# Kernel tuning notes

Measured on AMD Instinct MI355X. Metric: run time of the kernel, lower is better.

The kernel has to match this reference:

```python
import jax, jax.numpy as jnp
import numpy as np


def setup_inputs() -> dict:
    key = jax.random.key(0)
    ks = jax.random.split(key, 8)
    B, H, W, C = 4, 64, 64, 256
    Ck = C // 8  # key/query channels
    x = jax.random.normal(ks[0], (B, H, W, C), dtype=jnp.float32)
    Wf = jax.random.normal(ks[1], (C, Ck), dtype=jnp.float32) * (1.0 / np.sqrt(C))
    Wg = jax.random.normal(ks[2], (C, Ck), dtype=jnp.float32) * (1.0 / np.sqrt(C))
    Wh = jax.random.normal(ks[3], (C, C), dtype=jnp.float32) * (1.0 / np.sqrt(C))
    bf = jnp.zeros((Ck,), dtype=jnp.float32)
    bg = jnp.zeros((Ck,), dtype=jnp.float32)
    bh = jnp.zeros((C,), dtype=jnp.float32)
    gamma = jax.random.normal(ks[4], (), dtype=jnp.float32) * 0.1
    return {"x": x, "Wf": Wf, "bf": bf, "Wg": Wg, "bg": bg, "Wh": Wh, "bh": bh, "gamma": gamma}


def reference(x, Wf, bf, Wg, bg, Wh, bh, gamma):
    B, H, W, C = x.shape
    N = H * W
    # 1x1 convs == per-pixel matmuls over channel dim
    f = jnp.einsum('bhwc,ck->bhwk', x, Wf) + bf  # [B,H,W,C/8]
    g = jnp.einsum('bhwc,ck->bhwk', x, Wg) + bg  # [B,H,W,C/8]
    h = jnp.einsum('bhwc,cd->bhwd', x, Wh) + bh  # [B,H,W,C]
    f_flat = f.reshape(B, N, -1)
    g_flat = g.reshape(B, N, -1)
    h_flat = h.reshape(B, N, C)
    # s[b,i,j] = <g_i, f_j>   (query = g, key = f, as in the TF code)
    s = jnp.einsum('bik,bjk->bij', g_flat, f_flat)  # [B,N,N]
    b = jax.nn.softmax(s, axis=-1)
    o = jnp.einsum('bij,bjd->bid', b, h_flat)  # [B,N,C]
    y = gamma * o.reshape(B, H, W, C) + x
    return y
```

## Files before the change

kernel.cpp:

```cpp
#include <hip/hip_runtime.h>
#include <hip/hip_bf16.h>
#include <math.h>


typedef __bf16 bf16x8 __attribute__((ext_vector_type(8)));
typedef float f32x4 __attribute__((ext_vector_type(4)));

#define NPIX 4096
#define CDIM 256
#define CK   32

union U128 { unsigned int d[4]; uint4 u4; bf16x8 v; };

__device__ __forceinline__ unsigned int cvtpk(float lo, float hi) {
    unsigned int r;
    asm("v_cvt_pk_bf16_f32 %0, %1, %2" : "=v"(r) : "v"(lo), "v"(hi));
    return r;
}

__global__ __launch_bounds__(256) void prep_wtf(
    const float* __restrict__ Wf, const float* __restrict__ Wg,
    const float* __restrict__ Wh, __bf16* __restrict__ WTf)
{
    const int k = blockIdx.x;
    const int c = threadIdx.x;
    const int kk = k >> 5, kj = k & 31;
    {
        const float v = Wh[k * 256 + c];
        const int ct = 4 + (c >> 4), l15 = c & 15;
        WTf[((size_t)(ct * 8 + kk) * 16 + l15) * 32 + kj] = (__bf16)v;
    }
    if (c < 32) {
        const float v = Wf[k * 32 + c];
        const int ct = c >> 4, l15 = c & 15;
        WTf[((size_t)(ct * 8 + kk) * 16 + l15) * 32 + kj] = (__bf16)v;
    } else if (c < 64) {
        const int cc = c - 32;
        const float v = Wg[k * 32 + cc];
        const int ct = 2 + (cc >> 4), l15 = cc & 15;
        WTf[((size_t)(ct * 8 + kk) * 16 + l15) * 32 + kj] = (__bf16)v;
    }
}

__global__ __launch_bounds__(512, 1) void proj_mfma(
    const float* __restrict__ x, const __bf16* __restrict__ WTf,
    const float* __restrict__ bf_, const float* __restrict__ bg_,
    const float* __restrict__ bh_,
    __bf16* __restrict__ fbuf, __bf16* __restrict__ gbuf,
    __bf16* __restrict__ hT)
{
    __shared__ __bf16 xs[64 * 256];

    const int t = threadIdx.x;
    const int rowbase = blockIdx.x * 64;

    #pragma unroll
    for (int i = 0; i < 8; ++i) {
        const int flat = i * 2048 + t * 4;
        const int row = flat >> 8, col = flat & 255;
        const float4 xv = *(const float4*)&x[(size_t)rowbase * 256 + flat];
        const unsigned int d0 = cvtpk(xv.x, xv.y);
        const unsigned int d1 = cvtpk(xv.z, xv.w);
        const int s = (col >> 3) ^ (row & 7);
        uint2 w; w.x = d0; w.y = d1;
        *(uint2*)&xs[row * 256 + s * 8 + (col & 7)] = w;
    }
    __syncthreads();

    const int wv = t >> 6, lane = t & 63, l15 = lane & 15, lhi = lane >> 4;
    const int b = rowbase >> 12;
    const int nloc = rowbase & 4095;

    if (wv < 2) {
        const int rb0 = wv * 2;
        f32x4 acc[4][2];
        #pragma unroll
        for (int c = 0; c < 4; ++c)
            #pragma unroll
            for (int rb = 0; rb < 2; ++rb) acc[c][rb] = (f32x4){0.f, 0.f, 0.f, 0.f};
        #pragma unroll
        for (int kk = 0; kk < 8; ++kk) {
            bf16x8 xf[2];
            #pragma unroll
            for (int rb = 0; rb < 2; ++rb) {
                const int row = (rb0 + rb) * 16 + l15;
                xf[rb] = *(const bf16x8*)&xs[row * 256 + (((kk * 4 + lhi) ^ (row & 7)) * 8)];
            }
            #pragma unroll
            for (int c = 0; c < 4; ++c) {
                const bf16x8 w = *(const bf16x8*)&WTf[((size_t)(c * 8 + kk) * 16 + l15) * 32 + lhi * 8];
                acc[c][0] = __builtin_amdgcn_mfma_f32_16x16x32_bf16(xf[0], w, acc[c][0], 0, 0, 0);
                acc[c][1] = __builtin_amdgcn_mfma_f32_16x16x32_bf16(xf[1], w, acc[c][1], 0, 0, 0);
            }
        }
        #pragma unroll
        for (int c = 0; c < 4; ++c) {
            const float bia = (c < 2) ? bf_[c * 16 + l15] : bg_[(c - 2) * 16 + l15];
            __bf16* dst = (c < 2) ? fbuf : gbuf;
            const int ch = (c & 1) * 16 + l15;
            #pragma unroll
            for (int rb = 0; rb < 2; ++rb)
                #pragma unroll
                for (int r = 0; r < 4; ++r)
                    dst[(size_t)(rowbase + (rb0 + rb) * 16 + lhi * 4 + r) * CK + ch] =
                        (__bf16)(acc[c][rb][r] + bia);
        }
    } else {
        const int nct = (wv < 6) ? 3 : 2;
        const int ct0 = (wv < 6) ? (wv - 2) * 3 : 12 + (wv - 6) * 2;
        f32x4 acc[3][4];
        #pragma unroll
        for (int c = 0; c < 3; ++c)
            #pragma unroll
            for (int rb = 0; rb < 4; ++rb) acc[c][rb] = (f32x4){0.f, 0.f, 0.f, 0.f};
        #pragma unroll
        for (int kk = 0; kk < 8; ++kk) {
            bf16x8 xf[4];
            #pragma unroll
            for (int rb = 0; rb < 4; ++rb) {
                const int row = rb * 16 + l15;
                xf[rb] = *(const bf16x8*)&xs[row * 256 + (((kk * 4 + lhi) ^ (row & 7)) * 8)];
            }
            #pragma unroll
            for (int c = 0; c < 3; ++c) {
                if (c < nct) {
                    const bf16x8 w = *(const bf16x8*)
                        &WTf[((size_t)((4 + ct0 + c) * 8 + kk) * 16 + l15) * 32 + lhi * 8];
                    #pragma unroll
                    for (int rb = 0; rb < 4; ++rb)
                        acc[c][rb] = __builtin_amdgcn_mfma_f32_16x16x32_bf16(w, xf[rb], acc[c][rb], 0, 0, 0);
                }
            }
        }
        #pragma unroll
        for (int c = 0; c < 3; ++c) {
            if (c < nct) {
                #pragma unroll
                for (int r = 0; r < 4; ++r) {
                    const int ch = (ct0 + c) * 16 + lhi * 4 + r;
                    const float bia = bh_[ch];
                    #pragma unroll
                    for (int rb = 0; rb < 4; ++rb)
                        hT[((size_t)b * CDIM + ch) * NPIX + nloc + rb * 16 + l15] =
                            (__bf16)(acc[c][rb][r] + bia);
                }
            }
        }
    }
}

#define PL32(a, b) asm("v_permlane32_swap_b32 %0, %1" : "+v"(a), "+v"(b))
#define PL16(a, b) asm("v_permlane16_swap_b32 %0, %1" : "+v"(a), "+v"(b))

#define ATTN_TILE(KV, PB, FC, FN, HC, HN)                                           \
do {                                                                                \
    if (wv < 4) {                                                                   \
        const f32x4 m30 = {-30.f, -30.f, -30.f, -30.f};                             \
        f32x4 s0 = __builtin_amdgcn_mfma_f32_16x16x32_bf16(FC[0], ga, m30, 0, 0, 0);\
        f32x4 s1 = __builtin_amdgcn_mfma_f32_16x16x32_bf16(FC[1], ga, m30, 0, 0, 0);\
        f32x4 s2 = __builtin_amdgcn_mfma_f32_16x16x32_bf16(FC[2], ga, m30, 0, 0, 0);\
        f32x4 s3 = __builtin_amdgcn_mfma_f32_16x16x32_bf16(FC[3], ga, m30, 0, 0, 0);\
        {                                                 \
            const size_t ko = (size_t)((KV) + 64) * CK;                             \
            FN[0] = *(const bf16x8*)(fp + ko);                                      \
            FN[1] = *(const bf16x8*)(fp + ko + 16 * CK);                            \
            FN[2] = *(const bf16x8*)(fp + ko + 32 * CK);                            \
            FN[3] = *(const bf16x8*)(fp + ko + 48 * CK);                            \
        }                                                                           \
        float p0 = __expf(s0[0]), p1 = __expf(s0[1]), p2 = __expf(s0[2]), p3 = __expf(s0[3]); \
        float p4 = __expf(s1[0]), p5 = __expf(s1[1]), p6 = __expf(s1[2]), p7 = __expf(s1[3]); \
        float p8 = __expf(s2[0]), p9 = __expf(s2[1]), pa_ = __expf(s2[2]), pb_ = __expf(s2[3]); \
        float pc_ = __expf(s3[0]), pd_ = __expf(s3[1]), pe_ = __expf(s3[2]), pf_ = __expf(s3[3]); \
        lsum += ((p0 + p1) + (p2 + p3)) + ((p4 + p5) + (p6 + p7))                   \
              + ((p8 + p9) + (pa_ + pb_)) + ((pc_ + pd_) + (pe_ + pf_));            \
        unsigned int u0 = cvtpk(p0, p1), u1 = cvtpk(p2, p3);                        \
        unsigned int u2 = cvtpk(p4, p5), u3 = cvtpk(p6, p7);                        \
        unsigned int u4 = cvtpk(p8, p9), u5 = cvtpk(pa_, pb_);                      \
        unsigned int u6 = cvtpk(pc_, pd_), u7 = cvtpk(pe_, pf_);                    \
        PL32(u0, u2); PL32(u1, u3); PL32(u4, u6); PL32(u5, u7);                     \
        PL16(u0, u2); PL16(u1, u3); PL16(u4, u6); PL16(u5, u7);                     \
        uint4 w0; w0.x = u0; w0.y = u1; w0.z = u2; w0.w = u3;                       \
        uint4 w1; w1.x = u4; w1.y = u5; w1.z = u6; w1.w = u7;                       \
        pbuf[PB][wv * 2 + 0][lane] = w0;                                            \
        pbuf[PB][wv * 2 + 1][lane] = w1;                                            \
    }                                                                               \
    __syncthreads();                                                                \
    {                                                     \
        const size_t kn = (size_t)((KV) + 64);                                      \
        HN[0] = *(const bf16x8*)(hp + kn);                                          \
        HN[1] = *(const bf16x8*)(hp + kn + 32);                                     \
        if (wv >= 4) {                                                              \
            HN[2] = *(const bf16x8*)(hp + (size_t)16 * NPIX + kn);                  \
            HN[3] = *(const bf16x8*)(hp + (size_t)16 * NPIX + kn + 32);             \
            HN[4] = *(const bf16x8*)(hp + (size_t)32 * NPIX + kn);                  \
            HN[5] = *(const bf16x8*)(hp + (size_t)32 * NPIX + kn + 32);             \
        }                                                                           \
    }                                                                               \
    __builtin_amdgcn_s_setprio(1);                                                  \
    _Pragma("unroll")                                                               \
    for (int rt = 0; rt < 4; ++rt) {                                                \
        U128 A0, A1;                                                                \
        A0.u4 = pbuf[PB][rt * 2 + 0][lane];                                         \
        A1.u4 = pbuf[PB][rt * 2 + 1][lane];                                         \
        O_[rt][0] = __builtin_amdgcn_mfma_f32_16x16x32_bf16(A0.v, HC[0], O_[rt][0], 0, 0, 0); \
        O_[rt][0] = __builtin_amdgcn_mfma_f32_16x16x32_bf16(A1.v, HC[1], O_[rt][0], 0, 0, 0); \
        if (wv >= 4) {                                                              \
            O_[rt][1] = __builtin_amdgcn_mfma_f32_16x16x32_bf16(A0.v, HC[2], O_[rt][1], 0, 0, 0); \
            O_[rt][1] = __builtin_amdgcn_mfma_f32_16x16x32_bf16(A1.v, HC[3], O_[rt][1], 0, 0, 0); \
            O_[rt][2] = __builtin_amdgcn_mfma_f32_16x16x32_bf16(A0.v, HC[4], O_[rt][2], 0, 0, 0); \
            O_[rt][2] = __builtin_amdgcn_mfma_f32_16x16x32_bf16(A1.v, HC[5], O_[rt][2], 0, 0, 0); \
        }                                                                           \
    }                                                                               \
    __builtin_amdgcn_s_setprio(0);                                                  \
} while (0)

__global__ __launch_bounds__(512, 1) void attn_kernel(
    const __bf16* __restrict__ fbuf, const __bf16* __restrict__ gbuf,
    const __bf16* __restrict__ hT, const float* __restrict__ x,
    const float* __restrict__ gamma_p, float* __restrict__ out)
{
    __shared__ uint4 pbuf[2][8][64];
    __shared__ float lbuf[64];

    const int t = threadIdx.x;
    const int lane = t & 63;
    const int wv = t >> 6;
    const int l15 = lane & 15;
    const int lhi = lane >> 4;

    const int xcd = blockIdx.x & 7;
    const int b = xcd >> 1;
    const int qt = ((blockIdx.x >> 3) << 1) + (xcd & 1);
    const int q0 = qt * 64;

    const __bf16* fb = fbuf + (size_t)b * NPIX * CK;
    const __bf16* hb = hT + (size_t)b * CDIM * NPIX;

    const int dbase = (wv < 4) ? wv * 16 : 64 + (wv - 4) * 48;
    const __bf16* hp = hb + (size_t)(dbase + l15) * NPIX + lhi * 8;
    const __bf16* fp = fb + (size_t)l15 * CK + lhi * 8;

    bf16x8 ga = {};
    if (wv < 4)
        ga = *(const bf16x8*)&gbuf[((size_t)b * NPIX + q0 + wv * 16 + l15) * CK + lhi * 8];

    f32x4 O_[4][3];
    #pragma unroll
    for (int i = 0; i < 4; ++i)
        #pragma unroll
        for (int j = 0; j < 3; ++j) O_[i][j] = (f32x4){0.f, 0.f, 0.f, 0.f};
    float lsum = 0.f;

    bf16x8 FA[4], FB[4], HA[6], HB[6];

    if (wv < 4) {
        FA[0] = *(const bf16x8*)(fp);
        FA[1] = *(const bf16x8*)(fp + 16 * CK);
        FA[2] = *(const bf16x8*)(fp + 32 * CK);
        FA[3] = *(const bf16x8*)(fp + 48 * CK);
    }
    HA[0] = *(const bf16x8*)(hp);
    HA[1] = *(const bf16x8*)(hp + 32);
    if (wv >= 4) {
        HA[2] = *(const bf16x8*)(hp + (size_t)16 * NPIX);
        HA[3] = *(const bf16x8*)(hp + (size_t)16 * NPIX + 32);
        HA[4] = *(const bf16x8*)(hp + (size_t)32 * NPIX);
        HA[5] = *(const bf16x8*)(hp + (size_t)32 * NPIX + 32);
    }

    for (int it = 0; it < 32; ++it) {
        const int kv = it * 128;
        ATTN_TILE(kv,      0, FA, FB, HA, HB);
        ATTN_TILE(kv + 64, 1, FB, FA, HB, HA);
    }

    if (wv < 4) {
        lsum += __shfl_xor(lsum, 16, 64);
        lsum += __shfl_xor(lsum, 32, 64);
        if (lane < 16) lbuf[wv * 16 + l15] = lsum;
    }
    __syncthreads();

    const float gm = gamma_p[0];
    #pragma unroll
    for (int rt = 0; rt < 4; ++rt) {
        #pragma unroll
        for (int r = 0; r < 4; ++r) {
            const int row = rt * 16 + lhi * 4 + r;
            const float rl = gm / lbuf[row];
            const size_t base = ((size_t)b * NPIX + q0 + row) * CDIM + dbase;
            out[base + l15] = fmaf(rl, O_[rt][0][r], x[base + l15]);
            if (wv >= 4) {
                out[base + 16 + l15] = fmaf(rl, O_[rt][1][r], x[base + 16 + l15]);
                out[base + 32 + l15] = fmaf(rl, O_[rt][2][r], x[base + 32 + l15]);
            }
        }
    }
}

extern "C" void kernel_launch(void* const* d_in, const int* in_sizes, int n_in,
                              void* d_out, int out_size, void* d_ws, size_t ws_size,
                              hipStream_t stream)
{
    const float* x     = (const float*)d_in[0];
    const float* Wf    = (const float*)d_in[1];
    const float* bf    = (const float*)d_in[2];
    const float* Wg    = (const float*)d_in[3];
    const float* bg    = (const float*)d_in[4];
    const float* Wh    = (const float*)d_in[5];
    const float* bh    = (const float*)d_in[6];
    const float* gamma = (const float*)d_in[7];
    float* out = (float*)d_out;

    __bf16* fbuf = (__bf16*)d_ws;
    __bf16* gbuf = fbuf + (size_t)4 * NPIX * CK;
    __bf16* hT   = gbuf + (size_t)4 * NPIX * CK;
    __bf16* WTf  = hT + (size_t)4 * CDIM * NPIX;

    prep_wtf<<<256, 256, 0, stream>>>(Wf, Wg, Wh, WTf);
    proj_mfma<<<256, 512, 0, stream>>>(x, WTf, bf, bg, bh, fbuf, gbuf, hT);
    attn_kernel<<<256, 512, 0, stream>>>(fbuf, gbuf, hT, x, gamma, out);
}
```

Before: 182.3 us.

## Halve attention query tile to 32 rows and shrink projection blocks

The attention kernel now processes 32 queries per block with 4 waves: 2 waves compute scores/softmax, and all 4 waves accumulate wider output channel slices. The grid doubles to 512 blocks with launch bounds allowing 2 blocks per CU. The projection kernel uses 16-row blocks of 256 threads (1024 blocks), and the weight prep is re-indexed to coalesced writes. The syncthreads is replaced with an lgkmcnt wait plus s_barrier, and the KV prefetch index wraps to avoid out-of-bounds reads. More blocks improve CU fill and latency hiding, but each block now rereads all of f and hT, doubling K/V traffic per query, and per-wave register pressure increases.

```diff
diff --git a/kernel.cpp b/kernel.cpp
--- a/kernel.cpp
+++ b/kernel.cpp
@@ -22,129 +22,87 @@
     const float* __restrict__ Wf, const float* __restrict__ Wg,
     const float* __restrict__ Wh, __bf16* __restrict__ WTf)
 {
-    const int k = blockIdx.x;
-    const int c = threadIdx.x;
-    const int kk = k >> 5, kj = k & 31;
-    {
-        const float v = Wh[k * 256 + c];
-        const int ct = 4 + (c >> 4), l15 = c & 15;
-        WTf[((size_t)(ct * 8 + kk) * 16 + l15) * 32 + kj] = (__bf16)v;
-    }
-    if (c < 32) {
-        const float v = Wf[k * 32 + c];
-        const int ct = c >> 4, l15 = c & 15;
-        WTf[((size_t)(ct * 8 + kk) * 16 + l15) * 32 + kj] = (__bf16)v;
-    } else if (c < 64) {
-        const int cc = c - 32;
-        const float v = Wg[k * 32 + cc];
-        const int ct = 2 + (cc >> 4), l15 = cc & 15;
-        WTf[((size_t)(ct * 8 + kk) * 16 + l15) * 32 + kj] = (__bf16)v;
-    }
-}
-
-__global__ __launch_bounds__(512, 1) void proj_mfma(
+    const int idx = blockIdx.x * 256 + threadIdx.x;
+    const int j   = idx & 31;
+    const int l15 = (idx >> 5) & 15;
+    const int kk  = (idx >> 9) & 7;
+    const int ct  = idx >> 12;
+    const int k   = kk * 32 + j;
+    float v;
+    if (ct < 2)      v = Wf[k * 32 + ct * 16 + l15];
+    else if (ct < 4) v = Wg[k * 32 + (ct - 2) * 16 + l15];
+    else             v = Wh[k * 256 + (ct - 4) * 16 + l15];
+    WTf[idx] = (__bf16)v;
+}
+
+__global__ __launch_bounds__(256, 4) void proj_mfma(
     const float* __restrict__ x, const __bf16* __restrict__ WTf,
     const float* __restrict__ bf_, const float* __restrict__ bg_,
     const float* __restrict__ bh_,
     __bf16* __restrict__ fbuf, __bf16* __restrict__ gbuf,
     __bf16* __restrict__ hT)
 {
-    __shared__ __bf16 xs[64 * 256];
+    __shared__ __bf16 xs[16 * 256];
 
     const int t = threadIdx.x;
-    const int rowbase = blockIdx.x * 64;
-
-    #pragma unroll
-    for (int i = 0; i < 8; ++i) {
-        const int flat = i * 2048 + t * 4;
-        const int row = flat >> 8, col = flat & 255;
-        const float4 xv = *(const float4*)&x[(size_t)rowbase * 256 + flat];
-        const unsigned int d0 = cvtpk(xv.x, xv.y);
-        const unsigned int d1 = cvtpk(xv.z, xv.w);
-        const int s = (col >> 3) ^ (row & 7);
-        uint2 w; w.x = d0; w.y = d1;
-        *(uint2*)&xs[row * 256 + s * 8 + (col & 7)] = w;
+    const int rowbase = blockIdx.x * 16;
+
+    {
+        const int flat = t * 4;
+        #pragma unroll
+        for (int i = 0; i < 4; ++i) {
+            const int f2 = i * 1024 + flat;
+            const int row = f2 >> 8, col = f2 & 255;
+            const float4 xv = *(const float4*)&x[(size_t)rowbase * 256 + f2];
+            const unsigned int d0 = cvtpk(xv.x, xv.y);
+            const unsigned int d1 = cvtpk(xv.z, xv.w);
+            const int s = (col >> 3) ^ (row & 7);
+            uint2 w; w.x = d0; w.y = d1;
+            *(uint2*)&xs[row * 256 + s * 8 + (col & 7)] = w;
+        }
     }
     __syncthreads();
 
     const int wv = t >> 6, lane = t & 63, l15 = lane & 15, lhi = lane >> 4;
+
+    f32x4 acc[5];
+    #pragma unroll
+    for (int i = 0; i < 5; ++i) acc[i] = (f32x4){0.f, 0.f, 0.f, 0.f};
+
+    #pragma unroll 2
+    for (int kk = 0; kk < 8; ++kk) {
+        const bf16x8 xfrag =
+            *(const bf16x8*)&xs[l15 * 256 + (((kk * 4 + lhi) ^ (l15 & 7)) * 8)];
+        #pragma unroll
+        for (int j = 0; j < 5; ++j) {
+            const int ct = wv + j * 4;
+            const bf16x8 w =
+                *(const bf16x8*)&WTf[((size_t)(ct * 8 + kk) * 16 + l15) * 32 + lhi * 8];
+            if (j == 0)
+                acc[j] = __builtin_amdgcn_mfma_f32_16x16x32_bf16(xfrag, w, acc[j], 0, 0, 0);
+            else
+                acc[j] = __builtin_amdgcn_mfma_f32_16x16x32_bf16(w, xfrag, acc[j], 0, 0, 0);
+        }
+    }
+
     const int b = rowbase >> 12;
     const int nloc = rowbase & 4095;
-
-    if (wv < 2) {
-        const int rb0 = wv * 2;
-        f32x4 acc[4][2];
-        #pragma unroll
-        for (int c = 0; c < 4; ++c)
-            #pragma unroll
-            for (int rb = 0; rb < 2; ++rb) acc[c][rb] = (f32x4){0.f, 0.f, 0.f, 0.f};
-        #pragma unroll
-        for (int kk = 0; kk < 8; ++kk) {
-            bf16x8 xf[2];
-            #pragma unroll
-            for (int rb = 0; rb < 2; ++rb) {
-                const int row = (rb0 + rb) * 16 + l15;
-                xf[rb] = *(const bf16x8*)&xs[row * 256 + (((kk * 4 + lhi) ^ (row & 7)) * 8)];
-            }
-            #pragma unroll
-            for (int c = 0; c < 4; ++c) {
-                const bf16x8 w = *(const bf16x8*)&WTf[((size_t)(c * 8 + kk) * 16 + l15) * 32 + lhi * 8];
-                acc[c][0] = __builtin_amdgcn_mfma_f32_16x16x32_bf16(xf[0], w, acc[c][0], 0, 0, 0);
-                acc[c][1] = __builtin_amdgcn_mfma_f32_16x16x32_bf16(xf[1], w, acc[c][1], 0, 0, 0);
-            }
-        }
-        #pragma unroll
-        for (int c = 0; c < 4; ++c) {
-            const float bia = (c < 2) ? bf_[c * 16 + l15] : bg_[(c - 2) * 16 + l15];
-            __bf16* dst = (c < 2) ? fbuf : gbuf;
-            const int ch = (c & 1) * 16 + l15;
-            #pragma unroll
-            for (int rb = 0; rb < 2; ++rb)
-                #pragma unroll
-                for (int r = 0; r < 4; ++r)
-                    dst[(size_t)(rowbase + (rb0 + rb) * 16 + lhi * 4 + r) * CK + ch] =
-                        (__bf16)(acc[c][rb][r] + bia);
-        }
-    } else {
-        const int nct = (wv < 6) ? 3 : 2;
-        const int ct0 = (wv < 6) ? (wv - 2) * 3 : 12 + (wv - 6) * 2;
-        f32x4 acc[3][4];
-        #pragma unroll
-        for (int c = 0; c < 3; ++c)
-            #pragma unroll
-            for (int rb = 0; rb < 4; ++rb) acc[c][rb] = (f32x4){0.f, 0.f, 0.f, 0.f};
-        #pragma unroll
-        for (int kk = 0; kk < 8; ++kk) {
-            bf16x8 xf[4];
-            #pragma unroll
-            for (int rb = 0; rb < 4; ++rb) {
-                const int row = rb * 16 + l15;
-                xf[rb] = *(const bf16x8*)&xs[row * 256 + (((kk * 4 + lhi) ^ (row & 7)) * 8)];
-            }
-            #pragma unroll
-            for (int c = 0; c < 3; ++c) {
-                if (c < nct) {
-                    const bf16x8 w = *(const bf16x8*)
-                        &WTf[((size_t)((4 + ct0 + c) * 8 + kk) * 16 + l15) * 32 + lhi * 8];
-                    #pragma unroll
-                    for (int rb = 0; rb < 4; ++rb)
-                        acc[c][rb] = __builtin_amdgcn_mfma_f32_16x16x32_bf16(w, xf[rb], acc[c][rb], 0, 0, 0);
-                }
-            }
-        }
-        #pragma unroll
-        for (int c = 0; c < 3; ++c) {
-            if (c < nct) {
-                #pragma unroll
-                for (int r = 0; r < 4; ++r) {
-                    const int ch = (ct0 + c) * 16 + lhi * 4 + r;
-                    const float bia = bh_[ch];
-                    #pragma unroll
-                    for (int rb = 0; rb < 4; ++rb)
-                        hT[((size_t)b * CDIM + ch) * NPIX + nloc + rb * 16 + l15] =
-                            (__bf16)(acc[c][rb][r] + bia);
-                }
-            }
+    {
+        const int ct = wv;
+        const float bia = (ct < 2) ? bf_[(ct & 1) * 16 + l15] : bg_[(ct & 1) * 16 + l15];
+        __bf16* dst = (ct < 2) ? fbuf : gbuf;
+        const int ch = (ct & 1) * 16 + l15;
+        #pragma unroll
+        for (int r = 0; r < 4; ++r)
+            dst[(size_t)(rowbase + lhi * 4 + r) * CK + ch] = (__bf16)(acc[0][r] + bia);
+    }
+    #pragma unroll
+    for (int j = 1; j < 5; ++j) {
+        const int dtile = wv + (j - 1) * 4;
+        #pragma unroll
+        for (int r = 0; r < 4; ++r) {
+            const int d = dtile * 16 + lhi * 4 + r;
+            hT[((size_t)b * CDIM + d) * NPIX + nloc + l15] = (__bf16)(acc[j][r] + bh_[d]);
         }
     }
 }
@@ -154,14 +112,14 @@
 
 #define ATTN_TILE(KV, PB, FC, FN, HC, HN)                                           \
 do {                                                                                \
-    if (wv < 4) {                                                                   \
+    if (wv < 2) {                                                                   \
         const f32x4 m30 = {-30.f, -30.f, -30.f, -30.f};                             \
         f32x4 s0 = __builtin_amdgcn_mfma_f32_16x16x32_bf16(FC[0], ga, m30, 0, 0, 0);\
         f32x4 s1 = __builtin_amdgcn_mfma_f32_16x16x32_bf16(FC[1], ga, m30, 0, 0, 0);\
         f32x4 s2 = __builtin_amdgcn_mfma_f32_16x16x32_bf16(FC[2], ga, m30, 0, 0, 0);\
         f32x4 s3 = __builtin_amdgcn_mfma_f32_16x16x32_bf16(FC[3], ga, m30, 0, 0, 0);\
-        {                                                 \
-            const size_t ko = (size_t)((KV) + 64) * CK;                             \
+        {            \
+            const size_t ko = (size_t)(((KV) + 64) & 4095) * CK;                    \
             FN[0] = *(const bf16x8*)(fp + ko);                                      \
             FN[1] = *(const bf16x8*)(fp + ko + 16 * CK);                            \
             FN[2] = *(const bf16x8*)(fp + ko + 32 * CK);                            \
@@ -184,43 +142,50 @@
         pbuf[PB][wv * 2 + 0][lane] = w0;                                            \
         pbuf[PB][wv * 2 + 1][lane] = w1;                                            \
     }                                                                               \
-    __syncthreads();                                                                \
+                   \
+    asm volatile("s_waitcnt lgkmcnt(0)\n\ts_barrier" ::: "memory");                 \
     {                                                     \
-        const size_t kn = (size_t)((KV) + 64);                                      \
+        const size_t kn = (size_t)(((KV) + 64) & 4095);                             \
         HN[0] = *(const bf16x8*)(hp + kn);                                          \
         HN[1] = *(const bf16x8*)(hp + kn + 32);                                     \
-        if (wv >= 4) {                                                              \
-            HN[2] = *(const bf16x8*)(hp + (size_t)16 * NPIX + kn);                  \
-            HN[3] = *(const bf16x8*)(hp + (size_t)16 * NPIX + kn + 32);             \
-            HN[4] = *(const bf16x8*)(hp + (size_t)32 * NPIX + kn);                  \
-            HN[5] = *(const bf16x8*)(hp + (size_t)32 * NPIX + kn + 32);             \
+        HN[2] = *(const bf16x8*)(hp + (size_t)16 * NPIX + kn);                      \
+        HN[3] = *(const bf16x8*)(hp + (size_t)16 * NPIX + kn + 32);                 \
+        if (wv >= 2) {                                                              \
+            _Pragma("unroll")                                                       \
+            for (int dt = 2; dt < 6; ++dt) {                                        \
+                HN[dt * 2 + 0] = *(const bf16x8*)(hp + (size_t)dt * 16 * NPIX + kn);\
+                HN[dt * 2 + 1] = *(const bf16x8*)(hp + (size_t)dt * 16 * NPIX + kn + 32); \
+            }                                                                       \
         }                                                                           \
     }                                                                               \
     __builtin_amdgcn_s_setprio(1);                                                  \
     _Pragma("unroll")                                                               \
-    for (int rt = 0; rt < 4; ++rt) {                                                \
+    for (int rt = 0; rt < 2; ++rt) {                                                \
         U128 A0, A1;                                                                \
         A0.u4 = pbuf[PB][rt * 2 + 0][lane];                                         \
         A1.u4 = pbuf[PB][rt * 2 + 1][lane];                                         \
         O_[rt][0] = __builtin_amdgcn_mfma_f32_16x16x32_bf16(A0.v, HC[0], O_[rt][0], 0, 0, 0); \
         O_[rt][0] = __builtin_amdgcn_mfma_f32_16x16x32_bf16(A1.v, HC[1], O_[rt][0], 0, 0, 0); \
-        if (wv >= 4) {                                                              \
-            O_[rt][1] = __builtin_amdgcn_mfma_f32_16x16x32_bf16(A0.v, HC[2], O_[rt][1], 0, 0, 0); \
-            O_[rt][1] = __builtin_amdgcn_mfma_f32_16x16x32_bf16(A1.v, HC[3], O_[rt][1], 0, 0, 0); \
-            O_[rt][2] = __builtin_amdgcn_mfma_f32_16x16x32_bf16(A0.v, HC[4], O_[rt][2], 0, 0, 0); \
-            O_[rt][2] = __builtin_amdgcn_mfma_f32_16x16x32_bf16(A1.v, HC[5], O_[rt][2], 0, 0, 0); \
+        O_[rt][1] = __builtin_amdgcn_mfma_f32_16x16x32_bf16(A0.v, HC[2], O_[rt][1], 0, 0, 0); \
+        O_[rt][1] = __builtin_amdgcn_mfma_f32_16x16x32_bf16(A1.v, HC[3], O_[rt][1], 0, 0, 0); \
+        if (wv >= 2) {                                                              \
+            _Pragma("unroll")                                                       \
+            for (int dt = 2; dt < 6; ++dt) {                                        \
+                O_[rt][dt] = __builtin_amdgcn_mfma_f32_16x16x32_bf16(A0.v, HC[dt * 2 + 0], O_[rt][dt], 0, 0, 0); \
+                O_[rt][dt] = __builtin_amdgcn_mfma_f32_16x16x32_bf16(A1.v, HC[dt * 2 + 1], O_[rt][dt], 0, 0, 0); \
+            }                                                                       \
         }                                                                           \
     }                                                                               \
     __builtin_amdgcn_s_setprio(0);                                                  \
 } while (0)
 
-__global__ __launch_bounds__(512, 1) void attn_kernel(
+__global__ __launch_bounds__(256, 2) void attn_kernel(
     const __bf16* __restrict__ fbuf, const __bf16* __restrict__ gbuf,
     const __bf16* __restrict__ hT, const float* __restrict__ x,
     const float* __restrict__ gamma_p, float* __restrict__ out)
 {
-    __shared__ uint4 pbuf[2][8][64];
-    __shared__ float lbuf[64];
+    __shared__ uint4 pbuf[2][4][64];
+    __shared__ float lbuf[32];
 
     const int t = threadIdx.x;
     const int lane = t & 63;
@@ -231,29 +196,29 @@
     const int xcd = blockIdx.x & 7;
     const int b = xcd >> 1;
     const int qt = ((blockIdx.x >> 3) << 1) + (xcd & 1);
-    const int q0 = qt * 64;
+    const int q0 = qt * 32;
 
     const __bf16* fb = fbuf + (size_t)b * NPIX * CK;
     const __bf16* hb = hT + (size_t)b * CDIM * NPIX;
 
-    const int dbase = (wv < 4) ? wv * 16 : 64 + (wv - 4) * 48;
+    const int dbase = (wv < 2) ? wv * 32 : 64 + (wv - 2) * 96;
     const __bf16* hp = hb + (size_t)(dbase + l15) * NPIX + lhi * 8;
     const __bf16* fp = fb + (size_t)l15 * CK + lhi * 8;
 
     bf16x8 ga = {};
-    if (wv < 4)
+    if (wv < 2)
         ga = *(const bf16x8*)&gbuf[((size_t)b * NPIX + q0 + wv * 16 + l15) * CK + lhi * 8];
 
-    f32x4 O_[4][3];
-    #pragma unroll
-    for (int i = 0; i < 4; ++i)
-        #pragma unroll
-        for (int j = 0; j < 3; ++j) O_[i][j] = (f32x4){0.f, 0.f, 0.f, 0.f};
+    f32x4 O_[2][6];
+    #pragma unroll
+    for (int i = 0; i < 2; ++i)
+        #pragma unroll
+        for (int j = 0; j < 6; ++j) O_[i][j] = (f32x4){0.f, 0.f, 0.f, 0.f};
     float lsum = 0.f;
 
-    bf16x8 FA[4], FB[4], HA[6], HB[6];
-
-    if (wv < 4) {
+    bf16x8 FA[4], FB[4], HA[12], HB[12];
+
+    if (wv < 2) {
         FA[0] = *(const bf16x8*)(fp);
         FA[1] = *(const bf16x8*)(fp + 16 * CK);
         FA[2] = *(const bf16x8*)(fp + 32 * CK);
@@ -261,11 +226,14 @@
     }
     HA[0] = *(const bf16x8*)(hp);
     HA[1] = *(const bf16x8*)(hp + 32);
-    if (wv >= 4) {
-        HA[2] = *(const bf16x8*)(hp + (size_t)16 * NPIX);
-        HA[3] = *(const bf16x8*)(hp + (size_t)16 * NPIX + 32);
-        HA[4] = *(const bf16x8*)(hp + (size_t)32 * NPIX);
-        HA[5] = *(const bf16x8*)(hp + (size_t)32 * NPIX + 32);
+    HA[2] = *(const bf16x8*)(hp + (size_t)16 * NPIX);
+    HA[3] = *(const bf16x8*)(hp + (size_t)16 * NPIX + 32);
+    if (wv >= 2) {
+        #pragma unroll
+        for (int dt = 2; dt < 6; ++dt) {
+            HA[dt * 2 + 0] = *(const bf16x8*)(hp + (size_t)dt * 16 * NPIX);
+            HA[dt * 2 + 1] = *(const bf16x8*)(hp + (size_t)dt * 16 * NPIX + 32);
+        }
     }
 
     for (int it = 0; it < 32; ++it) {
@@ -274,7 +242,7 @@
         ATTN_TILE(kv + 64, 1, FB, FA, HB, HA);
     }
 
-    if (wv < 4) {
+    if (wv < 2) {
         lsum += __shfl_xor(lsum, 16, 64);
         lsum += __shfl_xor(lsum, 32, 64);
         if (lane < 16) lbuf[wv * 16 + l15] = lsum;
@@ -283,16 +251,19 @@
 
     const float gm = gamma_p[0];
     #pragma unroll
-    for (int rt = 0; rt < 4; ++rt) {
+    for (int rt = 0; rt < 2; ++rt) {
         #pragma unroll
         for (int r = 0; r < 4; ++r) {
             const int row = rt * 16 + lhi * 4 + r;
             const float rl = gm / lbuf[row];
             const size_t base = ((size_t)b * NPIX + q0 + row) * CDIM + dbase;
-            out[base + l15] = fmaf(rl, O_[rt][0][r], x[base + l15]);
-            if (wv >= 4) {
-                out[base + 16 + l15] = fmaf(rl, O_[rt][1][r], x[base + 16 + l15]);
-                out[base + 32 + l15] = fmaf(rl, O_[rt][2][r], x[base + 32 + l15]);
+            out[base + l15]      = fmaf(rl, O_[rt][0][r], x[base + l15]);
+            out[base + 16 + l15] = fmaf(rl, O_[rt][1][r], x[base + 16 + l15]);
+            if (wv >= 2) {
+                #pragma unroll
+                for (int dt = 2; dt < 6; ++dt)
+                    out[base + dt * 16 + l15] =
+                        fmaf(rl, O_[rt][dt][r], x[base + dt * 16 + l15]);
             }
         }
     }
@@ -317,7 +288,7 @@
     __bf16* hT   = gbuf + (size_t)4 * NPIX * CK;
     __bf16* WTf  = hT + (size_t)4 * CDIM * NPIX;
 
-    prep_wtf<<<256, 256, 0, stream>>>(Wf, Wg, Wh, WTf);
-    proj_mfma<<<256, 512, 0, stream>>>(x, WTf, bf, bg, bh, fbuf, gbuf, hT);
-    attn_kernel<<<256, 512, 0, stream>>>(fbuf, gbuf, hT, x, gamma, out);
-}
+    prep_wtf<<<320, 256, 0, stream>>>(Wf, Wg, Wh, WTf);
+    proj_mfma<<<1024, 256, 0, stream>>>(x, WTf, bf, bg, bh, fbuf, gbuf, hT);
+    attn_kernel<<<512, 256, 0, stream>>>(fbuf, gbuf, hT, x, gamma, out);
+}
```

Result: slower. 235.6 us (+29.2%).
